# Performance work log

Measured on AMD Instinct MI355X. Metric: run time of the kernel, lower is better.

The kernel has to match this reference:

```python
import jax, jax.numpy as jnp
import numpy as np

ALPHA = 0.25


def setup_inputs() -> dict:
    key = jax.random.key(0)
    pos_seq = jax.random.normal(key, (64, 8192, 51), dtype=jnp.float32)
    return {"pos_seq": pos_seq}


def _ema(pos_seq, alpha):
    # out[0] = x[0]; out[t] = alpha*x[t] + (1-alpha)*out[t-1]
    x0 = pos_seq[:, 0]                      # (B, D)
    xs = jnp.swapaxes(pos_seq[:, 1:], 0, 1)  # (T-1, B, D) for scan over time

    def step(carry, x_t):
        y = alpha * x_t + (1.0 - alpha) * carry
        return y, y

    _, ys = jax.lax.scan(step, x0, xs)      # ys: (T-1, B, D)
    ys = jnp.swapaxes(ys, 0, 1)             # (B, T-1, D)
    return jnp.concatenate([pos_seq[:, :1], ys], axis=1)


def reference(pos_seq):
    return _ema(pos_seq, ALPHA)
```

## Files before the change

### kernel.cpp

```cpp
#include <hip/hip_runtime.h>


typedef float vfloat4 __attribute__((ext_vector_type(4)));

#define T_DIM 8192
#define C_DIM 51
#define L_ROWS 128
#define H_ROWS 48
#define TILE_ROWS (L_ROWS + H_ROWS)
#define TILE_ELEMS (TILE_ROWS * C_DIM)
#define OUT_ELEMS (L_ROWS * C_DIM)
#define SUB_LEN 32
#define NSUB 4
#define NCHUNK (T_DIM / L_ROWS)

__global__ __launch_bounds__(256, 4) void ema_kernel(const float* __restrict__ x,
                                                     float* __restrict__ y) {
    __shared__ float tile[TILE_ELEMS];

    const int tid = threadIdx.x;
    const int chunk = blockIdx.x % NCHUNK;
    const int b = blockIdx.x / NCHUNK;
    const size_t plane = (size_t)b * ((size_t)T_DIM * C_DIM);
    const int t0 = chunk * L_ROWS;
    const int start_f = (t0 - H_ROWS) * C_DIM;

    const float* __restrict__ xp = x + plane;

    if (chunk != 0) {
        for (int j = tid; j < TILE_ELEMS / 4; j += 256) {
            vfloat4 v = *(const vfloat4*)(xp + start_f + 4 * j);
            *(vfloat4*)(&tile[4 * j]) = v;
        }
    } else {
        for (int j = tid; j < TILE_ELEMS / 4; j += 256) {
            int e = start_f + 4 * j;
            if (e >= 0) {
                *(vfloat4*)(&tile[4 * j]) = *(const vfloat4*)(xp + e);
            } else {
                vfloat4 v;
#pragma unroll
                for (int k = 0; k < 4; ++k) {
                    int c = (e + k + H_ROWS * C_DIM) % C_DIM;
                    v[k] = xp[c];
                }
                *(vfloat4*)(&tile[4 * j]) = v;
            }
        }
    }
    __syncthreads();

    const int c = tid % C_DIM;
    const int sub = tid / C_DIM;
    const bool active = (tid < NSUB * C_DIM);
    float acc = 0.0f;
    if (active) {
        const int tr = sub * SUB_LEN;
        acc = tile[tr * C_DIM + c];
#pragma unroll
        for (int i = 1; i < H_ROWS; ++i)
            acc = fmaf(0.25f, tile[(tr + i) * C_DIM + c], 0.75f * acc);
    }
    __syncthreads();

    if (active) {
        const int base = (H_ROWS + sub * SUB_LEN) * C_DIM + c;
#pragma unroll
        for (int i = 0; i < SUB_LEN; ++i) {
            float xv = tile[base + i * C_DIM];
            acc = fmaf(0.25f, xv, 0.75f * acc);
            tile[base + i * C_DIM] = acc;
        }
    }
    __syncthreads();

    float* __restrict__ yp = y + plane + (size_t)t0 * C_DIM;
    for (int j = tid; j < OUT_ELEMS / 4; j += 256) {
        vfloat4 v = *(const vfloat4*)(&tile[H_ROWS * C_DIM + 4 * j]);
        __builtin_nontemporal_store(v, (vfloat4*)(yp + 4 * j));
    }
}

extern "C" void kernel_launch(void* const* d_in, const int* in_sizes, int n_in,
                              void* d_out, int out_size, void* d_ws, size_t ws_size,
                              hipStream_t stream) {
    const float* x = (const float*)d_in[0];
    float* y = (float*)d_out;

    int B = in_sizes[0] / (T_DIM * C_DIM);
    int grid = B * NCHUNK;
    ema_kernel<<<grid, 256, 0, stream>>>(x, y);
}
```

Before: 190.4 us.

## Stream 256-row spans through single-wavefront blocks with register-prefetched tiles

Each block is now a single 64-lane wavefront that processes a 256-row span as four 64-row tiles. It prefetches the next tile into registers while running the sequential scan on the current tile in LDS, then stores the results. Warm-up shrinks to a single 64-row tile per span, replacing the earlier 48-row halo per 128-row chunk, so redundant reads go down. The risks are that only 51 of 64 lanes do the serial scan, each block runs a long serial chain, and occupancy per wave depends on 52 registers of prefetch state. The 64-row warm-up truncates the carry at 0.75^64, which is still negligible.

```diff
diff --git a/kernel.cpp b/kernel.cpp
--- a/kernel.cpp
+++ b/kernel.cpp
@@ -1,83 +1,90 @@
 #include <hip/hip_runtime.h>
 
 
-typedef float vfloat4 __attribute__((ext_vector_type(4)));
+typedef float vf4 __attribute__((ext_vector_type(4)));
 
 #define T_DIM 8192
 #define C_DIM 51
-#define L_ROWS 128
-#define H_ROWS 48
-#define TILE_ROWS (L_ROWS + H_ROWS)
-#define TILE_ELEMS (TILE_ROWS * C_DIM)
-#define OUT_ELEMS (L_ROWS * C_DIM)
-#define SUB_LEN 32
-#define NSUB 4
-#define NCHUNK (T_DIM / L_ROWS)
+#define TILE 64
+#define SPAN 256
+#define NSPAN (T_DIM / SPAN)
+#define NTILE (SPAN / TILE)
+#define TILE_F (TILE * C_DIM)
+#define TILE_V4 (TILE_F / 4)
+#define VPL 13
 
-__global__ __launch_bounds__(256, 4) void ema_kernel(const float* __restrict__ x,
-                                                     float* __restrict__ y) {
-    __shared__ float tile[TILE_ELEMS];
+__global__ __launch_bounds__(64) void ema_kernel(const float* __restrict__ x,
+                                                 float* __restrict__ y) {
+    __shared__ float buf[TILE_F];
 
-    const int tid = threadIdx.x;
-    const int chunk = blockIdx.x % NCHUNK;
-    const int b = blockIdx.x / NCHUNK;
+    const int lane = threadIdx.x;
+    const int sp = blockIdx.x % NSPAN;
+    const int b = blockIdx.x / NSPAN;
     const size_t plane = (size_t)b * ((size_t)T_DIM * C_DIM);
-    const int t0 = chunk * L_ROWS;
-    const int start_f = (t0 - H_ROWS) * C_DIM;
+    const int t0 = sp * SPAN;
+    const bool warm = (sp != 0);
+    const int ntiles = warm ? NTILE + 1 : NTILE;
+    const int first_row = warm ? (t0 - TILE) : t0;
 
-    const float* __restrict__ xp = x + plane;
+    const float* __restrict__ xp = x + plane + (size_t)first_row * C_DIM;
+    float* __restrict__ yp = y + plane + (size_t)t0 * C_DIM;
 
-    if (chunk != 0) {
-        for (int j = tid; j < TILE_ELEMS / 4; j += 256) {
-            vfloat4 v = *(const vfloat4*)(xp + start_f + 4 * j);
-            *(vfloat4*)(&tile[4 * j]) = v;
-        }
-    } else {
-        for (int j = tid; j < TILE_ELEMS / 4; j += 256) {
-            int e = start_f + 4 * j;
-            if (e >= 0) {
-                *(vfloat4*)(&tile[4 * j]) = *(const vfloat4*)(xp + e);
-            } else {
-                vfloat4 v;
+    vf4 st[VPL];
 #pragma unroll
-                for (int k = 0; k < 4; ++k) {
-                    int c = (e + k + H_ROWS * C_DIM) % C_DIM;
-                    v[k] = xp[c];
-                }
-                *(vfloat4*)(&tile[4 * j]) = v;
+    for (int i = 0; i < VPL; ++i) {
+        const int j = i * 64 + lane;
+        if (j < TILE_V4) st[i] = *(const vf4*)(xp + 4 * j);
+    }
+#pragma unroll
+    for (int i = 0; i < VPL; ++i) {
+        const int j = i * 64 + lane;
+        if (j < TILE_V4) *(vf4*)(&buf[4 * j]) = st[i];
+    }
+
+    float acc = 0.0f;
+    if (lane < C_DIM) acc = buf[lane];
+
+    for (int k = 0; k < ntiles; ++k) {
+        const bool has_next = (k + 1 < ntiles);
+
+        if (has_next) {
+            const float* __restrict__ xn = xp + (size_t)(k + 1) * TILE_F;
+#pragma unroll
+            for (int i = 0; i < VPL; ++i) {
+                const int j = i * 64 + lane;
+                if (j < TILE_V4) st[i] = *(const vf4*)(xn + 4 * j);
             }
         }
-    }
-    __syncthreads();
 
-    const int c = tid % C_DIM;
-    const int sub = tid / C_DIM;
-    const bool active = (tid < NSUB * C_DIM);
-    float acc = 0.0f;
-    if (active) {
-        const int tr = sub * SUB_LEN;
-        acc = tile[tr * C_DIM + c];
+        if (lane < C_DIM) {
 #pragma unroll
-        for (int i = 1; i < H_ROWS; ++i)
-            acc = fmaf(0.25f, tile[(tr + i) * C_DIM + c], 0.75f * acc);
-    }
-    __syncthreads();
+            for (int t = 0; t < TILE; ++t) {
+                const float xv = buf[t * C_DIM + lane];
+                acc = fmaf(0.75f, acc, 0.25f * xv);
+                buf[t * C_DIM + lane] = acc;
+            }
+        }
 
-    if (active) {
-        const int base = (H_ROWS + sub * SUB_LEN) * C_DIM + c;
+        const bool stored = (!warm) || (k > 0);
+        if (stored) {
+            float* __restrict__ yo = yp + (size_t)(warm ? (k - 1) : k) * TILE_F;
 #pragma unroll
-        for (int i = 0; i < SUB_LEN; ++i) {
-            float xv = tile[base + i * C_DIM];
-            acc = fmaf(0.25f, xv, 0.75f * acc);
-            tile[base + i * C_DIM] = acc;
+            for (int i = 0; i < VPL; ++i) {
+                const int j = i * 64 + lane;
+                if (j < TILE_V4) {
+                    vf4 v = *(const vf4*)(&buf[4 * j]);
+                    __builtin_nontemporal_store(v, (vf4*)(yo + 4 * j));
+                }
+            }
         }
-    }
-    __syncthreads();
 
-    float* __restrict__ yp = y + plane + (size_t)t0 * C_DIM;
-    for (int j = tid; j < OUT_ELEMS / 4; j += 256) {
-        vfloat4 v = *(const vfloat4*)(&tile[H_ROWS * C_DIM + 4 * j]);
-        __builtin_nontemporal_store(v, (vfloat4*)(yp + 4 * j));
+        if (has_next) {
+#pragma unroll
+            for (int i = 0; i < VPL; ++i) {
+                const int j = i * 64 + lane;
+                if (j < TILE_V4) *(vf4*)(&buf[4 * j]) = st[i];
+            }
+        }
     }
 }
 
@@ -88,6 +95,6 @@
     float* y = (float*)d_out;
 
     int B = in_sizes[0] / (T_DIM * C_DIM);
-    int grid = B * NCHUNK;
-    ema_kernel<<<grid, 256, 0, stream>>>(x, y);
+    int grid = B * NSPAN;
+    ema_kernel<<<grid, 64, 0, stream>>>(x, y);
 }
```

Measured after the change: 198.5 us. 4.2% more time.
